# Performance work log

Measured on AMD Instinct MI355X. Metric: run time of the kernel, lower is better.

Reference implementation:

```python
import jax, jax.numpy as jnp
import numpy as np

CARD = [3049, 10, 7, 3]
EMB = 16
HID = 64
COV = 10
B = 4096
S = 512
IN_DIM = 1 + COV + len(CARD) * EMB + 1  # 76


def setup_inputs() -> dict:
    key = jax.random.key(0)
    ks = jax.random.split(key, 12)
    target = jax.random.uniform(ks[0], (B, S), dtype=jnp.float32) * 100.0
    covariates = jax.random.normal(ks[1], (B, S, COV), dtype=jnp.float32)
    static_cats = jax.random.randint(ks[2], (B, len(CARD)), 0, 3)
    scale = jax.random.uniform(ks[3], (B, 1), dtype=jnp.float32) * 10.0 + 0.1
    emb0 = jax.random.normal(ks[4], (CARD[0], EMB), dtype=jnp.float32) * 0.1
    emb1 = jax.random.normal(ks[5], (CARD[1], EMB), dtype=jnp.float32) * 0.1
    emb2 = jax.random.normal(ks[6], (CARD[2], EMB), dtype=jnp.float32) * 0.1
    emb3 = jax.random.normal(ks[7], (CARD[3], EMB), dtype=jnp.float32) * 0.1
    w_ih = jax.random.normal(ks[8], (IN_DIM, 4 * HID), dtype=jnp.float32) / np.sqrt(IN_DIM)
    w_hh = jax.random.normal(ks[9], (HID, 4 * HID), dtype=jnp.float32) / np.sqrt(HID)
    bias = jnp.zeros((4 * HID,), dtype=jnp.float32)
    w_out = jax.random.normal(ks[10], (HID, 2), dtype=jnp.float32) / np.sqrt(HID)
    b_out = jnp.zeros((2,), dtype=jnp.float32)
    return dict(target=target, covariates=covariates, static_cats=static_cats,
                scale=scale, emb0=emb0, emb1=emb1, emb2=emb2, emb3=emb3,
                w_ih=w_ih, w_hh=w_hh, bias=bias, w_out=w_out, b_out=b_out)


def reference(target, covariates, static_cats, scale,
              emb0, emb1, emb2, emb3, w_ih, w_hh, bias, w_out, b_out):
    # static embedding concat: [B, 4*EMB]
    static_emb = jnp.concatenate([emb0[static_cats[:, 0]], emb1[static_cats[:, 1]],
                                  emb2[static_cats[:, 2]], emb3[static_cats[:, 3]]], axis=-1)
    log_scale = jnp.log1p(scale)                              # [B, 1]
    static_x = jnp.concatenate([static_emb, log_scale], -1)  # [B, 4*EMB+1]
    # teacher-forced previous scaled target: shifted target/scale, zero at t=0
    ps = target / jnp.maximum(scale, 1e-4)                    # [B, S]
    prev = jnp.concatenate([jnp.zeros_like(ps[:, :1]), ps[:, :-1]], axis=1)

    h0 = jnp.zeros((target.shape[0], w_hh.shape[0]), dtype=target.dtype)

    def step(carry, xs):
        h, c = carry
        p_t, cov_t = xs  # [B], [B, COV]
        x = jnp.concatenate([p_t[:, None], cov_t, static_x], axis=-1)  # [B, IN_DIM]
        gates = x @ w_ih + h @ w_hh + bias
        i, f, g, o = jnp.split(gates, 4, axis=-1)
        i = jax.nn.sigmoid(i)
        f = jax.nn.sigmoid(f)
        g = jnp.tanh(g)
        o = jax.nn.sigmoid(o)
        c = f * c + i * g
        h = o * jnp.tanh(c)
        raw = h @ w_out + b_out                    # [B, 2]
        mu_s = jax.nn.softplus(raw[:, 0]) + 1e-4   # [B]
        al = jax.nn.softplus(raw[:, 1]) + 1e-4     # [B]
        return (h, c), (mu_s, al)

    xs = (prev.T, jnp.swapaxes(covariates, 0, 1))  # time-major
    _, (mu_s, al) = jax.lax.scan(step, (h0, h0), xs)
    mus = mu_s.T * scale   # [B, S]
    alphas = al.T          # [B, S]
    return mus, alphas
```

## Files before the change

kernel.cpp:

```cpp
#include <hip/hip_runtime.h>

#define BB 4096
#define SS 512
#define NG 256
#define BT 16
#define NT 512
#define CH 32
#define HSTR 68
#define PSTR 16
#define SBSTR 264
#define OSTR 33

typedef __bf16 bf16_t;
typedef bf16_t bf16x8 __attribute__((ext_vector_type(8)));
typedef float  f32x4  __attribute__((ext_vector_type(4)));

__device__ __forceinline__ unsigned short f2bf(float x) {
    union { float f; unsigned u; } q{x};
    unsigned r = (q.u + 0x7fffu + ((q.u >> 16) & 1u)) >> 16;
    return (unsigned short)r;
}
__device__ __forceinline__ float bf2f(unsigned short s) {
    union { unsigned u; float f; } q{((unsigned)s) << 16};
    return q.f;
}
#define LOG2E 1.4426950408889634f
__device__ __forceinline__ float frcp_(float x)  { return __builtin_amdgcn_rcpf(x); }
__device__ __forceinline__ float fexp2_(float x) { return __builtin_amdgcn_exp2f(x); }
__device__ __forceinline__ float flog2_(float x) { return __builtin_amdgcn_logf(x); }
__device__ __forceinline__ float softplus_(float x){ return x > 20.0f ? x : 0.6931471805599453f * flog2_(1.0f + fexp2_(LOG2E * x)); }

__device__ __forceinline__ void bar_lgkm() {
    asm volatile("s_waitcnt lgkmcnt(0)\n\ts_barrier" ::: "memory");
}

__global__ __launch_bounds__(NT)
void deepar_kernel(const float* __restrict__ target, const float* __restrict__ cov,
                   const int* __restrict__ cats, const float* __restrict__ scale,
                   const float* __restrict__ emb0, const float* __restrict__ emb1,
                   const float* __restrict__ emb2, const float* __restrict__ emb3,
                   const float* __restrict__ w_ih, const float* __restrict__ w_hh,
                   const float* __restrict__ bias, const float* __restrict__ w_out,
                   const float* __restrict__ b_out, float* __restrict__ out)
{
    __shared__ __attribute__((aligned(16))) unsigned char smemA[2 * CH * BT * PSTR * 2];
    __shared__ __attribute__((aligned(16))) unsigned short hbuf[2][BT][HSTR];
    __shared__ float obuf[2][CH][OSTR];
    __shared__ float inv_s[BT], scl_s[BT];

    unsigned short* pcx   = (unsigned short*)smemA;
    float*          sbias = (float*)smemA;
    float*          sx    = (float*)(smemA + BT * SBSTR * 4);

    const int tid  = threadIdx.x;
    const int b0   = blockIdx.x * BT;
    const int lane = tid & 63;
    const int wv   = tid >> 6;
    const int qd   = lane >> 4;
    const int ln   = lane & 15;
    const bool is_compute = (wv < 4);
    const int tid2 = tid & 255;

    for (int i = tid; i < 2 * BT * HSTR; i += NT) ((unsigned short*)hbuf)[i] = 0;
    if (tid < BT) {
        float s = scale[b0 + tid];
        scl_s[tid] = s;
        inv_s[tid] = 1.0f / fmaxf(s, 1e-4f);
        sx[tid * 68 + 64] = log1pf(s);
    }
    if (tid < BT * 4) {
        int r = tid >> 2, e = tid & 3;
        int c = cats[(b0 + r) * 4 + e];
        const float* eb = (e == 0 ? emb0 : e == 1 ? emb1 : e == 2 ? emb2 : emb3);
        for (int j = 0; j < 16; ++j) sx[r * 68 + e * 16 + j] = eb[c * 16 + j];
    }
    __syncthreads();

    {
        const int n = tid & 255, half = tid >> 8;
        float bj = bias[n];
        float acc[8];
        #pragma unroll
        for (int r = 0; r < 8; ++r) acc[r] = bj;
        for (int k = 0; k < 65; ++k) {
            float w = w_ih[(11 + k) * NG + n];
            #pragma unroll
            for (int r = 0; r < 8; ++r) acc[r] += sx[(half * 8 + r) * 68 + k] * w;
        }
        #pragma unroll
        for (int r = 0; r < 8; ++r) sbias[(half * 8 + r) * SBSTR + n] = acc[r];
    }
    __syncthreads();

    bf16x8 bfrag[4][3];
    f32x4  sbf[4];
    if (is_compute) {
        #pragma unroll
        for (int ti = 0; ti < 4; ++ti) {
            const float gsc = (ti == 2) ? (-2.0f * LOG2E) : (-LOG2E);
            const int n = ln + 16 * (wv + 4 * ti);
            #pragma unroll
            for (int c = 0; c < 3; ++c) {
                #pragma unroll
                for (int j = 0; j < 8; ++j) {
                    int k = qd * 8 + 32 * c + j;
                    float w;
                    if (k < 64)                  w = w_hh[k * NG + n];
                    else if (k == 64 || k == 75) w = w_ih[n];
                    else if (k <= 74)            w = w_ih[(k - 64) * NG + n];
                    else                         w = 0.0f;
                    bfrag[ti][c][j] = (bf16_t)(w * gsc);
                }
            }
            #pragma unroll
            for (int r = 0; r < 4; ++r)
                sbf[ti][r] = sbias[(qd * 4 + r) * SBSTR + n] * gsc;
        }
    }

    bf16x8 wob0, wob1;
    f32x4  bC;
    float  scl4[4];
    #pragma unroll
    for (int j = 0; j < 8; ++j) {
        wob0[j] = (bf16_t)((ln < 2) ? w_out[(qd * 8 + j) * 2 + ln] : 0.0f);
        wob1[j] = (bf16_t)((ln < 2) ? w_out[(32 + qd * 8 + j) * 2 + ln] : 0.0f);
    }
    #pragma unroll
    for (int r = 0; r < 4; ++r) {
        bC[r]   = (ln < 2) ? b_out[ln] : 0.0f;
        scl4[r] = (ln == 0) ? scl_s[qd * 4 + r] : 1.0f;
    }

    __syncthreads();

    for (int i = tid; i < (2 * CH * BT * PSTR) / 2; i += NT) ((int*)smemA)[i] = 0;
    __syncthreads();

    if (tid < 256) {
        const int row = tid >> 4, i5 = tid & 15;
        const float* cr = cov + (size_t)(b0 + row) * (SS * 10);
        #pragma unroll
        for (int j = 0; j < 20; ++j) {
            int e = i5 + 16 * j, tp = e / 10, k = e - 10 * tp;
            pcx[((0 * CH + tp) * BT + row) * PSTR + 1 + k] = f2bf(cr[e]);
        }
        float pv0 = (i5 == 0) ? 0.0f : target[(size_t)(b0 + row) * SS + i5 - 1] * inv_s[row];
        float pv1 = target[(size_t)(b0 + row) * SS + i5 + 15] * inv_s[row];
        unsigned short m0 = f2bf(pv0), m1 = f2bf(pv1);
        pcx[((0 * CH + i5) * BT + row) * PSTR + 0]       = m0;
        pcx[((0 * CH + i5) * BT + row) * PSTR + 11]      = f2bf(pv0 - bf2f(m0));
        pcx[((0 * CH + i5 + 16) * BT + row) * PSTR + 0]  = m1;
        pcx[((0 * CH + i5 + 16) * BT + row) * PSTR + 11] = f2bf(pv1 - bf2f(m1));
    }
    __syncthreads();

    bf16x8 a2 = {};
    f32x4 acc_pre[4];
    if (is_compute) {
        if (qd < 2)
            a2 = *(const bf16x8*)&pcx[((0 * CH + 0) * BT + ln) * PSTR + qd * 8];
        #pragma unroll
        for (int ti = 0; ti < 4; ++ti)
            acc_pre[ti] = __builtin_amdgcn_mfma_f32_16x16x32_bf16(a2, bfrag[ti][2], sbf[ti], 0, 0, 0);
        __builtin_amdgcn_s_setprio(1);
    }

    float cst[4] = {0.0f, 0.0f, 0.0f, 0.0f};
    float crg[20];
    #pragma unroll
    for (int j = 0; j < 20; ++j) crg[j] = 0.0f;
    float trg0 = 0.0f, trg1 = 0.0f;

    for (int t = 0; t < SS; ++t) {
        const int cur = t & 1, nxt = cur ^ 1;
        bar_lgkm();

        if (is_compute) {
            const unsigned short* hb = &hbuf[cur][ln][0];
            bf16x8 a0 = *(const bf16x8*)(hb + qd * 8);
            bf16x8 a1 = *(const bf16x8*)(hb + 32 + qd * 8);

            f32x4 acc0 = __builtin_amdgcn_mfma_f32_16x16x32_bf16(a0, bfrag[0][0], acc_pre[0], 0, 0, 0);
            f32x4 acc1 = __builtin_amdgcn_mfma_f32_16x16x32_bf16(a0, bfrag[1][0], acc_pre[1], 0, 0, 0);
            f32x4 acc2 = __builtin_amdgcn_mfma_f32_16x16x32_bf16(a0, bfrag[2][0], acc_pre[2], 0, 0, 0);
            f32x4 acc3 = __builtin_amdgcn_mfma_f32_16x16x32_bf16(a0, bfrag[3][0], acc_pre[3], 0, 0, 0);
            acc0 = __builtin_amdgcn_mfma_f32_16x16x32_bf16(a1, bfrag[0][1], acc0, 0, 0, 0);
            acc1 = __builtin_amdgcn_mfma_f32_16x16x32_bf16(a1, bfrag[1][1], acc1, 0, 0, 0);
            acc2 = __builtin_amdgcn_mfma_f32_16x16x32_bf16(a1, bfrag[2][1], acc2, 0, 0, 0);
            acc3 = __builtin_amdgcn_mfma_f32_16x16x32_bf16(a1, bfrag[3][1], acc3, 0, 0, 0);

            if (t + 1 < SS && qd < 2)
                a2 = *(const bf16x8*)&pcx[((((t + 1) >> 5) & 1) * CH + ((t + 1) & 31)) * BT * PSTR
                                          + ln * PSTR + qd * 8];

            const int u = 16 * wv + ln;
            #pragma unroll
            for (int r = 0; r < 4; ++r) {
                float si = frcp_(1.0f + fexp2_(acc0[r]));
                float sf = frcp_(1.0f + fexp2_(acc1[r]));
                float tg = 2.0f * frcp_(1.0f + fexp2_(acc2[r])) - 1.0f;
                float so = frcp_(1.0f + fexp2_(acc3[r]));
                float cc = sf * cst[r] + si * tg;
                cst[r] = cc;
                float th = 2.0f * frcp_(1.0f + fexp2_((-2.0f * LOG2E) * cc)) - 1.0f;
                *(bf16_t*)&hbuf[nxt][qd * 4 + r][u] = (bf16_t)(so * th);
            }

            if (t + 1 < SS) {
                #pragma unroll
                for (int ti = 0; ti < 4; ++ti)
                    acc_pre[ti] = __builtin_amdgcn_mfma_f32_16x16x32_bf16(a2, bfrag[ti][2], sbf[ti], 0, 0, 0);
            }
        } else {
            if ((t & 31) == 0 && t < 480) {
                const int row = tid2 >> 4, i5 = tid2 & 15, t0n = t + CH;
                const float* cr = cov + (size_t)(b0 + row) * (SS * 10) + t0n * 10;
                #pragma unroll
                for (int j = 0; j < 20; ++j) crg[j] = cr[i5 + 16 * j];
                const float* tr = target + (size_t)(b0 + row) * SS + t0n + i5;
                trg0 = tr[-1];
                trg1 = tr[15];
            }

            if (wv == 4 && t > 0) {
                const unsigned short* hb = &hbuf[cur][ln][0];
                bf16x8 a0 = *(const bf16x8*)(hb + qd * 8);
                bf16x8 a1 = *(const bf16x8*)(hb + 32 + qd * 8);
                f32x4 hacc = __builtin_amdgcn_mfma_f32_16x16x32_bf16(a0, wob0, bC, 0, 0, 0);
                hacc = __builtin_amdgcn_mfma_f32_16x16x32_bf16(a1, wob1, hacc, 0, 0, 0);
                if (ln < 2) {
                    #pragma unroll
                    for (int r = 0; r < 4; ++r) {
                        float sp = softplus_(hacc[r]) + 1e-4f;
                        obuf[((t - 1) >> 5) & 1][(t - 1) & 31][ln * 16 + qd * 4 + r] = sp * scl4[r];
                    }
                }
            }

            if ((t & 31) == 16) {
                const int c = t >> 5;
                if (c < 15) {
                    const int row = tid2 >> 4, i5 = tid2 & 15, nb = (c + 1) & 1;
                    float pv0 = trg0 * inv_s[row];
                    float pv1 = trg1 * inv_s[row];
                    unsigned short m0 = f2bf(pv0), m1 = f2bf(pv1);
                    pcx[((nb * CH + i5) * BT + row) * PSTR + 0]       = m0;
                    pcx[((nb * CH + i5) * BT + row) * PSTR + 11]      = f2bf(pv0 - bf2f(m0));
                    pcx[((nb * CH + i5 + 16) * BT + row) * PSTR + 0]  = m1;
                    pcx[((nb * CH + i5 + 16) * BT + row) * PSTR + 11] = f2bf(pv1 - bf2f(m1));
                    #pragma unroll
                    for (int j = 0; j < 20; ++j) {
                        int e = i5 + 16 * j, tp = e / 10, k = e - 10 * tp;
                        pcx[((nb * CH + tp) * BT + row) * PSTR + 1 + k] = f2bf(crg[j]);
                    }
                }
                if (c >= 1) {
                    const int pb = (c - 1) & 1, t0p = (c - 1) << 5;
                    #pragma unroll
                    for (int h = 0; h < 4; ++h) {
                        int e = tid2 + 256 * h;
                        int tte = e & 31, rowe = (e >> 5) & 15, pe = e >> 9;
                        out[(pe ? (BB * SS) : 0) + (size_t)(b0 + rowe) * SS + t0p + tte] =
                            obuf[pb][tte][pe * 16 + rowe];
                    }
                }
            }
        }
    }

    __syncthreads();
    if (wv == 4) {
        const unsigned short* hb = &hbuf[0][ln][0];
        bf16x8 a0 = *(const bf16x8*)(hb + qd * 8);
        bf16x8 a1 = *(const bf16x8*)(hb + 32 + qd * 8);
        f32x4 hacc = __builtin_amdgcn_mfma_f32_16x16x32_bf16(a0, wob0, bC, 0, 0, 0);
        hacc = __builtin_amdgcn_mfma_f32_16x16x32_bf16(a1, wob1, hacc, 0, 0, 0);
        if (ln < 2) {
            #pragma unroll
            for (int r = 0; r < 4; ++r) {
                float sp = softplus_(hacc[r]) + 1e-4f;
                obuf[1][31][ln * 16 + qd * 4 + r] = sp * scl4[r];
            }
        }
    }
    __syncthreads();
    #pragma unroll
    for (int h = 0; h < 2; ++h) {
        int e = tid + NT * h;
        int tte = e & 31, rowe = (e >> 5) & 15, pe = e >> 9;
        out[(pe ? (BB * SS) : 0) + (size_t)(b0 + rowe) * SS + 480 + tte] =
            obuf[1][tte][pe * 16 + rowe];
    }
}

extern "C" void kernel_launch(void* const* d_in, const int* in_sizes, int n_in,
                              void* d_out, int out_size, void* d_ws, size_t ws_size,
                              hipStream_t stream) {
    deepar_kernel<<<BB / BT, NT, 0, stream>>>(
        (const float*)d_in[0], (const float*)d_in[1], (const int*)d_in[2],
        (const float*)d_in[3], (const float*)d_in[4], (const float*)d_in[5],
        (const float*)d_in[6], (const float*)d_in[7], (const float*)d_in[8],
        (const float*)d_in[9], (const float*)d_in[10], (const float*)d_in[11],
        (const float*)d_in[12], (float*)d_out);
}
```

Measured before the change: 496.3 us.

## Transpose MFMA operand order so each lane packs its hidden-state write into one vector

Swaps the A/B operands of all gate and output-head MFMAs so the accumulator is transposed: each lane now holds 4 consecutive hidden units for one batch row. The new h value is then written to shared memory as a single bf16x4 store instead of four scattered 2-byte stores, and the bias, output-bias and scale mappings are adjusted to match. It also removes the s_setprio raise on the compute waves and moves the next-chunk staging from step 16 to step 8 of each chunk. Together these aim to shorten the per-timestep critical path of the serial recurrence, at the cost of a changed scheduling-priority balance between compute and loader waves.

```diff
diff --git a/kernel.cpp b/kernel.cpp
--- a/kernel.cpp
+++ b/kernel.cpp
@@ -13,6 +13,7 @@
 
 typedef __bf16 bf16_t;
 typedef bf16_t bf16x8 __attribute__((ext_vector_type(8)));
+typedef bf16_t bf16x4 __attribute__((ext_vector_type(4)));
 typedef float  f32x4  __attribute__((ext_vector_type(4)));
 
 __device__ __forceinline__ unsigned short f2bf(float x) {
@@ -114,23 +115,21 @@
             }
             #pragma unroll
             for (int r = 0; r < 4; ++r)
-                sbf[ti][r] = sbias[(qd * 4 + r) * SBSTR + n] * gsc;
+                sbf[ti][r] = sbias[ln * SBSTR + (16 * (wv + 4 * ti) + qd * 4 + r)] * gsc;
         }
     }
 
     bf16x8 wob0, wob1;
     f32x4  bC;
-    float  scl4[4];
     #pragma unroll
     for (int j = 0; j < 8; ++j) {
         wob0[j] = (bf16_t)((ln < 2) ? w_out[(qd * 8 + j) * 2 + ln] : 0.0f);
         wob1[j] = (bf16_t)((ln < 2) ? w_out[(32 + qd * 8 + j) * 2 + ln] : 0.0f);
     }
     #pragma unroll
-    for (int r = 0; r < 4; ++r) {
-        bC[r]   = (ln < 2) ? b_out[ln] : 0.0f;
-        scl4[r] = (ln == 0) ? scl_s[qd * 4 + r] : 1.0f;
-    }
+    for (int r = 0; r < 4; ++r)
+        bC[r] = (qd == 0 && r < 2) ? b_out[r] : 0.0f;
+    const float sclh = scl_s[ln];
 
     __syncthreads();
 
@@ -162,8 +161,7 @@
             a2 = *(const bf16x8*)&pcx[((0 * CH + 0) * BT + ln) * PSTR + qd * 8];
         #pragma unroll
         for (int ti = 0; ti < 4; ++ti)
-            acc_pre[ti] = __builtin_amdgcn_mfma_f32_16x16x32_bf16(a2, bfrag[ti][2], sbf[ti], 0, 0, 0);
-        __builtin_amdgcn_s_setprio(1);
+            acc_pre[ti] = __builtin_amdgcn_mfma_f32_16x16x32_bf16(bfrag[ti][2], a2, sbf[ti], 0, 0, 0);
     }
 
     float cst[4] = {0.0f, 0.0f, 0.0f, 0.0f};
@@ -181,20 +179,20 @@
             bf16x8 a0 = *(const bf16x8*)(hb + qd * 8);
             bf16x8 a1 = *(const bf16x8*)(hb + 32 + qd * 8);
 
-            f32x4 acc0 = __builtin_amdgcn_mfma_f32_16x16x32_bf16(a0, bfrag[0][0], acc_pre[0], 0, 0, 0);
-            f32x4 acc1 = __builtin_amdgcn_mfma_f32_16x16x32_bf16(a0, bfrag[1][0], acc_pre[1], 0, 0, 0);
-            f32x4 acc2 = __builtin_amdgcn_mfma_f32_16x16x32_bf16(a0, bfrag[2][0], acc_pre[2], 0, 0, 0);
-            f32x4 acc3 = __builtin_amdgcn_mfma_f32_16x16x32_bf16(a0, bfrag[3][0], acc_pre[3], 0, 0, 0);
-            acc0 = __builtin_amdgcn_mfma_f32_16x16x32_bf16(a1, bfrag[0][1], acc0, 0, 0, 0);
-            acc1 = __builtin_amdgcn_mfma_f32_16x16x32_bf16(a1, bfrag[1][1], acc1, 0, 0, 0);
-            acc2 = __builtin_amdgcn_mfma_f32_16x16x32_bf16(a1, bfrag[2][1], acc2, 0, 0, 0);
-            acc3 = __builtin_amdgcn_mfma_f32_16x16x32_bf16(a1, bfrag[3][1], acc3, 0, 0, 0);
+            f32x4 acc0 = __builtin_amdgcn_mfma_f32_16x16x32_bf16(bfrag[0][0], a0, acc_pre[0], 0, 0, 0);
+            f32x4 acc1 = __builtin_amdgcn_mfma_f32_16x16x32_bf16(bfrag[1][0], a0, acc_pre[1], 0, 0, 0);
+            f32x4 acc2 = __builtin_amdgcn_mfma_f32_16x16x32_bf16(bfrag[2][0], a0, acc_pre[2], 0, 0, 0);
+            f32x4 acc3 = __builtin_amdgcn_mfma_f32_16x16x32_bf16(bfrag[3][0], a0, acc_pre[3], 0, 0, 0);
+            acc0 = __builtin_amdgcn_mfma_f32_16x16x32_bf16(bfrag[0][1], a1, acc0, 0, 0, 0);
+            acc1 = __builtin_amdgcn_mfma_f32_16x16x32_bf16(bfrag[1][1], a1, acc1, 0, 0, 0);
+            acc2 = __builtin_amdgcn_mfma_f32_16x16x32_bf16(bfrag[2][1], a1, acc2, 0, 0, 0);
+            acc3 = __builtin_amdgcn_mfma_f32_16x16x32_bf16(bfrag[3][1], a1, acc3, 0, 0, 0);
 
             if (t + 1 < SS && qd < 2)
                 a2 = *(const bf16x8*)&pcx[((((t + 1) >> 5) & 1) * CH + ((t + 1) & 31)) * BT * PSTR
                                           + ln * PSTR + qd * 8];
 
-            const int u = 16 * wv + ln;
+            bf16x4 hq;
             #pragma unroll
             for (int r = 0; r < 4; ++r) {
                 float si = frcp_(1.0f + fexp2_(acc0[r]));
@@ -204,13 +202,14 @@
                 float cc = sf * cst[r] + si * tg;
                 cst[r] = cc;
                 float th = 2.0f * frcp_(1.0f + fexp2_((-2.0f * LOG2E) * cc)) - 1.0f;
-                *(bf16_t*)&hbuf[nxt][qd * 4 + r][u] = (bf16_t)(so * th);
-            }
+                hq[r] = (bf16_t)(so * th);
+            }
+            *(bf16x4*)&hbuf[nxt][ln][16 * wv + qd * 4] = hq;
 
             if (t + 1 < SS) {
                 #pragma unroll
                 for (int ti = 0; ti < 4; ++ti)
-                    acc_pre[ti] = __builtin_amdgcn_mfma_f32_16x16x32_bf16(a2, bfrag[ti][2], sbf[ti], 0, 0, 0);
+                    acc_pre[ti] = __builtin_amdgcn_mfma_f32_16x16x32_bf16(bfrag[ti][2], a2, sbf[ti], 0, 0, 0);
             }
         } else {
             if ((t & 31) == 0 && t < 480) {
@@ -227,18 +226,17 @@
                 const unsigned short* hb = &hbuf[cur][ln][0];
                 bf16x8 a0 = *(const bf16x8*)(hb + qd * 8);
                 bf16x8 a1 = *(const bf16x8*)(hb + 32 + qd * 8);
-                f32x4 hacc = __builtin_amdgcn_mfma_f32_16x16x32_bf16(a0, wob0, bC, 0, 0, 0);
-                hacc = __builtin_amdgcn_mfma_f32_16x16x32_bf16(a1, wob1, hacc, 0, 0, 0);
-                if (ln < 2) {
-                    #pragma unroll
-                    for (int r = 0; r < 4; ++r) {
-                        float sp = softplus_(hacc[r]) + 1e-4f;
-                        obuf[((t - 1) >> 5) & 1][(t - 1) & 31][ln * 16 + qd * 4 + r] = sp * scl4[r];
-                    }
+                f32x4 hacc = __builtin_amdgcn_mfma_f32_16x16x32_bf16(wob0, a0, bC, 0, 0, 0);
+                hacc = __builtin_amdgcn_mfma_f32_16x16x32_bf16(wob1, a1, hacc, 0, 0, 0);
+                if (qd == 0) {
+                    float sp0 = softplus_(hacc[0]) + 1e-4f;
+                    float sp1 = softplus_(hacc[1]) + 1e-4f;
+                    obuf[((t - 1) >> 5) & 1][(t - 1) & 31][ln]      = sp0 * sclh;
+                    obuf[((t - 1) >> 5) & 1][(t - 1) & 31][16 + ln] = sp1;
                 }
             }
 
-            if ((t & 31) == 16) {
+            if ((t & 31) == 8) {
                 const int c = t >> 5;
                 if (c < 15) {
                     const int row = tid2 >> 4, i5 = tid2 & 15, nb = (c + 1) & 1;
@@ -255,6 +253,10 @@
                         pcx[((nb * CH + tp) * BT + row) * PSTR + 1 + k] = f2bf(crg[j]);
                     }
                 }
+            }
+
+            if ((t & 31) == 16) {
+                const int c = t >> 5;
                 if (c >= 1) {
                     const int pb = (c - 1) & 1, t0p = (c - 1) << 5;
                     #pragma unroll
@@ -274,14 +276,13 @@
         const unsigned short* hb = &hbuf[0][ln][0];
         bf16x8 a0 = *(const bf16x8*)(hb + qd * 8);
         bf16x8 a1 = *(const bf16x8*)(hb + 32 + qd * 8);
-        f32x4 hacc = __builtin_amdgcn_mfma_f32_16x16x32_bf16(a0, wob0, bC, 0, 0, 0);
-        hacc = __builtin_amdgcn_mfma_f32_16x16x32_bf16(a1, wob1, hacc, 0, 0, 0);
-        if (ln < 2) {
-            #pragma unroll
-            for (int r = 0; r < 4; ++r) {
-                float sp = softplus_(hacc[r]) + 1e-4f;
-                obuf[1][31][ln * 16 + qd * 4 + r] = sp * scl4[r];
-            }
+        f32x4 hacc = __builtin_amdgcn_mfma_f32_16x16x32_bf16(wob0, a0, bC, 0, 0, 0);
+        hacc = __builtin_amdgcn_mfma_f32_16x16x32_bf16(wob1, a1, hacc, 0, 0, 0);
+        if (qd == 0) {
+            float sp0 = softplus_(hacc[0]) + 1e-4f;
+            float sp1 = softplus_(hacc[1]) + 1e-4f;
+            obuf[1][31][ln]      = sp0 * sclh;
+            obuf[1][31][16 + ln] = sp1;
         }
     }
     __syncthreads();
```

Result: no change. 490.2 us (-1.2%).
